# Kernel tuning notes

Hardware: AMD Instinct MI355X
Metric: run time of the kernel (lower is better)

Reference implementation:

```python
import jax, jax.numpy as jnp
import numpy as np

N_HEADS = 32
EPS = 1e-7
ROPE_BASE = 10000.0


def rms_norm(x, gamma):
    return x / jnp.sqrt(EPS + jnp.mean(x * x, axis=-1, keepdims=True)) * gamma


def rope_tables(seq_len, head_dim, dtype=jnp.float32):
    inv_freq = 1.0 / (ROPE_BASE ** (jnp.arange(0, head_dim, 2, dtype=jnp.float32) / head_dim))
    angles = jnp.arange(seq_len, dtype=jnp.float32)[:, None] * inv_freq[None, :]  # [S, D/2]
    angles = jnp.concatenate([angles, angles], axis=-1)  # [S, D]
    return jnp.cos(angles).astype(dtype), jnp.sin(angles).astype(dtype)


def apply_rope(x, cos, sin):
    # x: [B, H, S, D]; cos/sin: [S, D]
    d = x.shape[-1]
    x1, x2 = x[..., : d // 2], x[..., d // 2 :]
    rotated = jnp.concatenate([-x2, x1], axis=-1)
    return x * cos[None, None] + rotated * sin[None, None]


def setup_inputs() -> dict:
    key = jax.random.key(0)
    ks = jax.random.split(key, 9)
    B, S, D, Hd = 1, 2048, 4096, 11008
    s = lambda k, shape, fan: jax.random.normal(k, shape, jnp.float32) * (fan ** -0.5)
    return {
        "X": jax.random.normal(ks[0], (B, S, D), jnp.float32),
        "Wq": s(ks[1], (D, D), D),
        "Wk": s(ks[2], (D, D), D),
        "Wv": s(ks[3], (D, D), D),
        "Wo": s(ks[4], (D, D), D),
        "bo": jnp.zeros((D,), jnp.float32),
        "gamma1": jnp.ones((D,), jnp.float32),
        "gamma2": jnp.ones((D,), jnp.float32),
        "W1": s(ks[5], (D, Hd), D),
        "W2": s(ks[6], (D, Hd), D),
        "W3": s(ks[7], (Hd, D), Hd),
    }


def reference(X, Wq, Wk, Wv, Wo, bo, gamma1, gamma2, W1, W2, W3):
    B, S, D = X.shape
    H = N_HEADS
    hd = D // H

    # --- attention sublayer ---
    h = rms_norm(X, gamma1)
    q = (h @ Wq).reshape(B, S, H, hd).transpose(0, 2, 1, 3)  # [B,H,S,hd]
    k = (h @ Wk).reshape(B, S, H, hd).transpose(0, 2, 1, 3)
    v = (h @ Wv).reshape(B, S, H, hd).transpose(0, 2, 1, 3)

    cos, sin = rope_tables(S, hd, X.dtype)
    q = apply_rope(q, cos, sin)
    k = apply_rope(k, cos, sin)

    scores = jnp.einsum("bhsd,bhtd->bhst", q, k) / jnp.sqrt(jnp.asarray(hd, X.dtype))
    causal = jnp.tril(jnp.ones((S, S), bool))
    scores = jnp.where(causal, scores, -jnp.inf)
    attn = jax.nn.softmax(scores, axis=-1)
    out = jnp.einsum("bhst,bhtd->bhsd", attn, v)
    out = out.transpose(0, 2, 1, 3).reshape(B, S, D)
    out = out @ Wo + bo
    X = X + out

    # --- SwiGLU FFN sublayer ---
    h2 = rms_norm(X, gamma2)
    x1 = h2 @ W1
    x2 = h2 @ W2
    ff = (x1 * jax.nn.sigmoid(x1) * x2) @ W3
    return X + ff
```

## Files before the change

### kernel.cpp

```cpp
#include <hip/hip_runtime.h>
#include <hip/hip_bf16.h>
#include <cstdint>
#include <cmath>

typedef __bf16 bf16;
typedef __attribute__((ext_vector_type(8))) __bf16 bf16x8;
typedef __attribute__((ext_vector_type(4))) __bf16 bf16x4;
typedef __attribute__((ext_vector_type(4))) float f32x4;

__device__ __forceinline__ void gload_lds16(const void* g, void* l) {
  __builtin_amdgcn_global_load_lds((__attribute__((address_space(1))) void*)g,
                                   (__attribute__((address_space(3))) void*)l,
                                   16, 0, 0);
}

template<int EPI>
__global__ __launch_bounds__(512, 2) void gemmd(
    const bf16* __restrict__ A, const bf16* __restrict__ Bt, void* __restrict__ Cv,
    const float* __restrict__ cosT, const float* __restrict__ sinT,
    bf16* __restrict__ q_out, bf16* __restrict__ k_out, bf16* __restrict__ v_out,
    int M, int N, int K, int ksd, int gm) {
  extern __shared__ char lds[];
  constexpr int BM = 256;
  constexpr int ASZ = BM * 128;
  constexpr int BUFS = ASZ + 32768;
  constexpr int MF = 4;

  const int tid = threadIdx.x;
  const int wave = tid >> 6, lane = tid & 63;
  const int wr = wave >> 1, wc = wave & 1;
  const int l15 = lane & 15, l4 = lane >> 4;
  const int qq = gridDim.x >> 3;
  const int wgid = (blockIdx.x & 7) * qq + (blockIdx.x >> 3);
  const int tm = wgid % gm;
  int tq = wgid / gm;
  int split = 0;
  if (EPI == 5) { split = tq / (N >> 8); tq = tq % (N >> 8); }
  const int tn = tq;
  const long brow = (long)tm * BM, bcol = (long)tn * 256;
  const long koff = (long)split * K;
  const int NT = K >> 6;
  const bf16* Ab = A + brow * ksd + koff;
  const bf16* Bb = Bt + bcol * ksd + koff;

  f32x4 acc[MF][8];
  #pragma unroll
  for (int i = 0; i < MF; ++i)
    #pragma unroll
    for (int j = 0; j < 8; ++j) acc[i][j] = (f32x4){0.f, 0.f, 0.f, 0.f};

  bf16x8 a[MF][2], b[8][2];

  auto stage = [&](int T) {
    const long kofs = (long)T << 6;
    char* wb = lds + (T & 1) * BUFS;
    #pragma unroll
    for (int i = 0; i < 4; ++i) {
      const int slot = i * 512 + tid, r = slot >> 3, c0 = slot & 7;
      gload_lds16(Ab + (long)r * ksd + kofs + ((c0 ^ (r & 7)) << 3), wb + slot * 16);
    }
    #pragma unroll
    for (int i = 0; i < 4; ++i) {
      const int slot = i * 512 + tid, r = slot >> 3, c0 = slot & 7;
      gload_lds16(Bb + (long)r * ksd + kofs + ((c0 ^ (r & 7)) << 3), wb + ASZ + slot * 16);
    }
  };

  stage(0);
  __syncthreads();

  for (int g = 0; g < NT; ++g) {
    const int pg = (g & 1) * BUFS;
    if (g + 1 < NT) stage(g + 1);
    #pragma unroll
    for (int nf = 0; nf < 8; ++nf)
      #pragma unroll
      for (int ks = 0; ks < 2; ++ks) {
        const int r = wc * 128 + nf * 16 + l15;
        b[nf][ks] = *(const bf16x8*)(lds + pg + ASZ + r * 128 + (((ks * 4 + l4) ^ (r & 7)) << 4));
      }
    #pragma unroll
    for (int mf = 0; mf < MF; ++mf)
      #pragma unroll
      for (int ks = 0; ks < 2; ++ks) {
        const int r = wr * 64 + mf * 16 + l15;
        a[mf][ks] = *(const bf16x8*)(lds + pg + r * 128 + (((ks * 4 + l4) ^ (r & 7)) << 4));
      }
    #pragma unroll
    for (int ks = 0; ks < 2; ++ks)
      #pragma unroll
      for (int mf = 0; mf < MF; ++mf)
        #pragma unroll
        for (int nf = 0; nf < 8; ++nf)
          acc[mf][nf] = __builtin_amdgcn_mfma_f32_16x16x32_bf16(
              a[mf][ks], b[nf][ks], acc[mf][nf], 0, 0, 0);
    __syncthreads();
  }

  if (EPI == 5) {
    bf16* dst = (split == 0 ? q_out : v_out);
    #pragma unroll
    for (int mf = 0; mf < MF; ++mf) {
      const long row0 = brow + wr * 64 + mf * 16 + l4 * 4;
      #pragma unroll
      for (int nf = 0; nf < 8; ++nf) {
        const long col = bcol + wc * 128 + nf * 16 + l15;
        #pragma unroll
        for (int rj = 0; rj < 4; ++rj)
          dst[(row0 + rj) * N + col] = (bf16)acc[mf][nf][rj];
      }
    }
  } else if (EPI == 3) {
    const int region = (int)(bcol >> 12);
    const int hc = (int)(bcol & 4095) + wc * 128;
    const int h = hc >> 7;
    if (region < 2) {
      bf16* dh = (region == 0 ? q_out : k_out) + (long)h * 2048 * 128;
      #pragma unroll
      for (int mf = 0; mf < MF; ++mf) {
        #pragma unroll
        for (int rj = 0; rj < 4; ++rj) {
          const int s = (int)brow + wr * 64 + mf * 16 + l4 * 4 + rj;
          const float* cr = cosT + s * 64;
          const float* sr = sinT + s * 64;
          #pragma unroll
          for (int nfp = 0; nfp < 4; ++nfp) {
            const int d = nfp * 16 + l15;
            const float c = cr[d], sn = sr[d];
            const float x1 = acc[mf][nfp][rj], x2 = acc[mf][nfp + 4][rj];
            dh[(long)s * 128 + d]      = (bf16)(x1 * c - x2 * sn);
            dh[(long)s * 128 + d + 64] = (bf16)(x2 * c + x1 * sn);
          }
        }
      }
    } else {
      bf16* dh = v_out + (long)h * 128 * 2048;
      #pragma unroll
      for (int mf = 0; mf < MF; ++mf) {
        const int s0 = (int)brow + wr * 64 + mf * 16 + l4 * 4;
        #pragma unroll
        for (int nf = 0; nf < 8; ++nf) {
          const int d = nf * 16 + l15;
          bf16x4 v;
          #pragma unroll
          for (int rj = 0; rj < 4; ++rj) v[rj] = (bf16)acc[mf][nf][rj];
          *(bf16x4*)(dh + (long)d * 2048 + s0) = v;
        }
      }
    }
  } else if (EPI == 4) {
    #pragma unroll
    for (int mf = 0; mf < MF; ++mf) {
      #pragma unroll
      for (int rj = 0; rj < 4; ++rj) {
        const int s = (int)brow + wr * 64 + mf * 16 + l4 * 4 + rj;
        bf16* gr = (bf16*)Cv + (long)s * 11008;
        #pragma unroll
        for (int nfp = 0; nfp < 4; ++nfp) {
          const int col = (int)bcol + wc * 128 + nfp * 32 + l15;
          const int jj = ((col >> 5) << 4) + l15;
          const float x1 = acc[mf][2 * nfp][rj], x2 = acc[mf][2 * nfp + 1][rj];
          const float sg = x1 / (1.f + __expf(-x1));
          gr[jj] = (bf16)(sg * x2);
        }
      }
    }
  }
}

__global__ __launch_bounds__(256) void combine_kernel(
    const bf16* __restrict__ p0, const bf16* __restrict__ p1,
    const float* __restrict__ X2, float* __restrict__ out) {
  const long i = ((long)blockIdx.x * 256 + threadIdx.x) * 8;
  bf16x8 a = *(const bf16x8*)(p0 + i);
  bf16x8 b = *(const bf16x8*)(p1 + i);
  #pragma unroll
  for (int j = 0; j < 8; ++j)
    out[i + j] = (float)a[j] + (float)b[j] + X2[i + j];
}

__global__ __launch_bounds__(256) void combine_wo_kernel(
    const bf16* __restrict__ p0, const bf16* __restrict__ p1,
    const float* __restrict__ bo, const float* __restrict__ X,
    const float* __restrict__ g2, float* __restrict__ X2,
    bf16* __restrict__ h2) {
  const int row = blockIdx.x;
  const long base = (long)row * 4096;
  float v[16];
  float ss = 0.f;
  #pragma unroll
  for (int c = 0; c < 2; ++c) {
    const int col = threadIdx.x * 8 + c * 2048;
    bf16x8 a = *(const bf16x8*)(p0 + base + col);
    bf16x8 b = *(const bf16x8*)(p1 + base + col);
    #pragma unroll
    for (int j = 0; j < 8; ++j) {
      const float val = (float)a[j] + (float)b[j] + bo[col + j] + X[base + col + j];
      v[c * 8 + j] = val;
      ss += val * val;
      X2[base + col + j] = val;
    }
  }
  #pragma unroll
  for (int off = 32; off; off >>= 1) ss += __shfl_down(ss, off, 64);
  __shared__ float wsum[4];
  if ((threadIdx.x & 63) == 0) wsum[threadIdx.x >> 6] = ss;
  __syncthreads();
  const float tot = wsum[0] + wsum[1] + wsum[2] + wsum[3];
  const float scale = rsqrtf(1e-7f + tot / 4096.f);
  #pragma unroll
  for (int c = 0; c < 2; ++c) {
    const int col = threadIdx.x * 8 + c * 2048;
    bf16x8 o;
    #pragma unroll
    for (int j = 0; j < 8; ++j)
      o[j] = (bf16)(v[c * 8 + j] * scale * g2[col + j]);
    *(bf16x8*)(h2 + base + col) = o;
  }
}

__device__ __forceinline__ void trans64(
    const float* __restrict__ in, bf16* __restrict__ out,
    int R, int C, int bx, int by, int ilv, int off) {
  __shared__ float t[64][65];
  const int lr = threadIdx.x >> 4;
  const int lc4 = (threadIdx.x & 15) * 4;
  #pragma unroll
  for (int i = 0; i < 4; ++i) {
    const int r = lr + i * 16;
    const float4 v = *(const float4*)(in + (long)(by * 64 + r) * C + bx * 64 + lc4);
    t[r][lc4] = v.x; t[r][lc4 + 1] = v.y; t[r][lc4 + 2] = v.z; t[r][lc4 + 3] = v.w;
  }
  __syncthreads();
  const int oc = threadIdx.x >> 4;
  const int or4 = (threadIdx.x & 15) * 4;
  #pragma unroll
  for (int i = 0; i < 4; ++i) {
    const int c = oc + i * 16;
    const int j = bx * 64 + c;
    const int rdst = ilv ? (((j >> 4) << 5) + off + (j & 15)) : j;
    bf16x4 v;
    #pragma unroll
    for (int k = 0; k < 4; ++k) v[k] = (bf16)t[or4 + k][c];
    *(bf16x4*)(out + (long)rdst * R + by * 64 + or4) = v;
  }
}

__global__ __launch_bounds__(256) void prep_kernel(
    const float* __restrict__ Wq, const float* __restrict__ Wk,
    const float* __restrict__ Wv, const float* __restrict__ Wo,
    const float* __restrict__ W1, const float* __restrict__ W2,
    const float* __restrict__ W3, const float* __restrict__ X,
    const float* __restrict__ g1,
    bf16* __restrict__ WqkvT, bf16* __restrict__ WoT,
    bf16* __restrict__ W12T, bf16* __restrict__ W3T,
    float* __restrict__ cosT, float* __restrict__ sinT,
    bf16* __restrict__ hbuf) {
  const int bid = blockIdx.x;
  if (bid < 16384) {
    const int seg = bid >> 12, idx = bid & 4095;
    const float* in = (seg == 0 ? Wq : seg == 1 ? Wk : seg == 2 ? Wv : Wo);
    bf16* out = (seg == 3 ? WoT : WqkvT + (long)seg * 4096 * 4096);
    trans64(in, out, 4096, 4096, idx & 63, idx >> 6, 0, 0);
  } else if (bid < 38400) {
    const int idx = bid - 16384;
    const int seg = idx / 11008, li = idx % 11008;
    trans64(seg ? W2 : W1, W12T, 4096, 11008, li % 172, li / 172, 1, seg * 16);
  } else if (bid < 49408) {
    const int idx = bid - 38400;
    trans64(W3, W3T, 11008, 4096, idx & 63, idx >> 6, 0, 0);
  } else if (bid < 49920) {
    const int gidx = (bid - 49408) * 256 + threadIdx.x;
    const int i = gidx & 63, s = gidx >> 6;
    const float inv = powf(10000.f, -(float)i / 64.f);
    const float ang = (float)s * inv;
    cosT[gidx] = cosf(ang);
    sinT[gidx] = sinf(ang);
  } else {
    const int row = bid - 49920;
    const float* xr = X + (long)row * 4096;
    float ss = 0.f;
    for (int i = threadIdx.x * 4; i < 4096; i += 1024) {
      float4 v = *(const float4*)(xr + i);
      ss += v.x * v.x + v.y * v.y + v.z * v.z + v.w * v.w;
    }
    #pragma unroll
    for (int off = 32; off; off >>= 1) ss += __shfl_down(ss, off, 64);
    __shared__ float wsum[4];
    if ((threadIdx.x & 63) == 0) wsum[threadIdx.x >> 6] = ss;
    __syncthreads();
    const float tot = wsum[0] + wsum[1] + wsum[2] + wsum[3];
    const float scale = rsqrtf(1e-7f + tot / 4096.f);
    bf16* orow = hbuf + (long)row * 4096;
    for (int i = threadIdx.x * 4; i < 4096; i += 1024) {
      float4 v = *(const float4*)(xr + i);
      float4 g = *(const float4*)(g1 + i);
      orow[i]     = (bf16)(v.x * scale * g.x);
      orow[i + 1] = (bf16)(v.y * scale * g.y);
      orow[i + 2] = (bf16)(v.z * scale * g.z);
      orow[i + 3] = (bf16)(v.w * scale * g.w);
    }
  }
}

__global__ __launch_bounds__(256) void attn_kernel(
    const bf16* __restrict__ qh, const bf16* __restrict__ kh,
    const bf16* __restrict__ vt, bf16* __restrict__ outb) {
  constexpr int S = 2048;
  const int qb = blockIdx.x, head = blockIdx.y;
  const int tid = threadIdx.x, wave = tid >> 6, lane = tid & 63;
  __shared__ bf16 Ks[2][64 * 128];
  __shared__ bf16 Vs[2][128 * 64];
  __shared__ bf16 Plds[4][16 * 64];
  const bf16* qhh = qh + (long)head * S * 128;
  const bf16* khh = kh + (long)head * S * 128;
  const bf16* vth = vt + (long)head * 128 * S;

  const int l15 = lane & 15, l4 = lane >> 4;
  const int qrow = qb * 64 + wave * 16 + l15;
  bf16x8 qf[4];
  #pragma unroll
  for (int kf = 0; kf < 4; ++kf)
    qf[kf] = *(const bf16x8*)(qhh + (long)qrow * 128 + kf * 32 + l4 * 8);

  auto stageKV = [&](int tb, int buf) {
    #pragma unroll
    for (int i = 0; i < 4; ++i) {
      const int c = wave + 4 * i;
      const int krlow = (c & 3) * 4 + l4;
      gload_lds16(khh + (long)(tb * 64 + c * 4 + l4) * 128 + ((l15 ^ krlow) * 8),
                  Ks[buf] + c * 512);
      gload_lds16(vth + (long)(c * 8 + (lane >> 3)) * S + tb * 64 +
                      (((lane & 7) ^ (lane >> 3)) * 8),
                  Vs[buf] + c * 512);
    }
  };

  float m_r[4], l_r[4];
  #pragma unroll
  for (int r = 0; r < 4; ++r) { m_r[r] = -INFINITY; l_r[r] = 0.f; }
  f32x4 oacc[8] = {};
  const float scale = 0.08838834764831845f;

  stageKV(0, 0);
  __syncthreads();

  for (int tb = 0; tb <= qb; ++tb) {
    const int buf = tb & 1;
    if (tb < qb) stageKV(tb + 1, buf ^ 1);

    f32x4 sf[4];
    #pragma unroll
    for (int ft = 0; ft < 4; ++ft) {
      f32x4 acn = {};
      #pragma unroll
      for (int kf = 0; kf < 4; ++kf) {
        bf16x8 kfr = *(const bf16x8*)(Ks[buf] + (ft * 16 + l15) * 128 +
                                      (((kf * 4 + l4) ^ l15) * 8));
        acn = __builtin_amdgcn_mfma_f32_16x16x32_bf16(qf[kf], kfr, acn, 0, 0, 0);
      }
      #pragma unroll
      for (int r = 0; r < 4; ++r) sf[ft][r] = acn[r] * scale;
    }
    if (tb == qb) {
      #pragma unroll
      for (int ft = 0; ft < 4; ++ft) {
        const int t_l = ft * 16 + l15;
        #pragma unroll
        for (int r = 0; r < 4; ++r)
          if (t_l > wave * 16 + l4 * 4 + r) sf[ft][r] = -INFINITY;
      }
    }
    float scl[4];
    #pragma unroll
    for (int r = 0; r < 4; ++r) {
      float mx = fmaxf(fmaxf(sf[0][r], sf[1][r]), fmaxf(sf[2][r], sf[3][r]));
      mx = fmaxf(mx, __shfl_xor(mx, 1, 64));
      mx = fmaxf(mx, __shfl_xor(mx, 2, 64));
      mx = fmaxf(mx, __shfl_xor(mx, 4, 64));
      mx = fmaxf(mx, __shfl_xor(mx, 8, 64));
      const float mnew = fmaxf(m_r[r], mx);
      scl[r] = __expf(m_r[r] - mnew);
      m_r[r] = mnew;
      float rs = 0.f;
      #pragma unroll
      for (int ft = 0; ft < 4; ++ft) {
        const float pexp = __expf(sf[ft][r] - mnew);
        sf[ft][r] = pexp;
        rs += pexp;
      }
      rs += __shfl_xor(rs, 1, 64);
      rs += __shfl_xor(rs, 2, 64);
      rs += __shfl_xor(rs, 4, 64);
      rs += __shfl_xor(rs, 8, 64);
      l_r[r] = l_r[r] * scl[r] + rs;
    }
    #pragma unroll
    for (int ft = 0; ft < 4; ++ft)
      #pragma unroll
      for (int r = 0; r < 4; ++r) {
        const int q = l4 * 4 + r;
        const int sl = (ft * 2 + (l15 >> 3)) ^ (q & 7);
        Plds[wave][q * 64 + sl * 8 + (l15 & 7)] = (bf16)sf[ft][r];
      }
    #pragma unroll
    for (int fd = 0; fd < 8; ++fd)
      #pragma unroll
      for (int r = 0; r < 4; ++r) oacc[fd][r] *= scl[r];
    #pragma unroll
    for (int fd = 0; fd < 8; ++fd) {
      #pragma unroll
      for (int kt = 0; kt < 2; ++kt) {
        bf16x8 pa = *(const bf16x8*)(&Plds[wave][l15 * 64 +
                        (((kt * 4 + l4) ^ (l15 & 7)) * 8)]);
        bf16x8 vb = *(const bf16x8*)(Vs[buf] + (fd * 16 + l15) * 64 +
                        (((kt * 4 + l4) ^ (l15 & 7)) * 8));
        oacc[fd] = __builtin_amdgcn_mfma_f32_16x16x32_bf16(pa, vb, oacc[fd], 0, 0, 0);
      }
    }
    __syncthreads();
  }
  #pragma unroll
  for (int fd = 0; fd < 8; ++fd) {
    #pragma unroll
    for (int r = 0; r < 4; ++r) {
      const long row = qb * 64 + wave * 16 + l4 * 4 + r;
      outb[row * 4096 + head * 128 + fd * 16 + l15] = (bf16)(oacc[fd][r] / l_r[r]);
    }
  }
}

extern "C" void kernel_launch(void* const* d_in, const int* in_sizes, int n_in,
                              void* d_out, int out_size, void* d_ws, size_t ws_size,
                              hipStream_t stream) {
  const float* X  = (const float*)d_in[0];
  const float* Wq = (const float*)d_in[1];
  const float* Wk = (const float*)d_in[2];
  const float* Wv = (const float*)d_in[3];
  const float* Wo = (const float*)d_in[4];
  const float* bo = (const float*)d_in[5];
  const float* g1 = (const float*)d_in[6];
  const float* g2 = (const float*)d_in[7];
  const float* W1 = (const float*)d_in[8];
  const float* W2 = (const float*)d_in[9];
  const float* W3 = (const float*)d_in[10];
  float* out = (float*)d_out;

  hipFuncSetAttribute((const void*)gemmd<3>, hipFuncAttributeMaxDynamicSharedMemorySize, 131072);
  hipFuncSetAttribute((const void*)gemmd<4>, hipFuncAttributeMaxDynamicSharedMemorySize, 131072);
  hipFuncSetAttribute((const void*)gemmd<5>, hipFuncAttributeMaxDynamicSharedMemorySize, 131072);

  char* p = (char*)d_ws;
  auto alloc = [&](size_t bytes) {
    char* r = p;
    p += (bytes + 255) & ~(size_t)255;
    return r;
  };
  float* cosT = (float*)alloc(2048 * 64 * 4);
  float* sinT = (float*)alloc(2048 * 64 * 4);
  bf16* WqkvT = (bf16*)alloc(12288L * 4096 * 2);
  bf16* WoT  = (bf16*)alloc(4096L * 4096 * 2);
  bf16* W12T = (bf16*)alloc(22016L * 4096 * 2);
  bf16* W3T  = (bf16*)alloc(4096L * 11008 * 2);
  bf16* qhB  = (bf16*)alloc(2048L * 4096 * 2);
  bf16* khB  = (bf16*)alloc(2048L * 4096 * 2);
  bf16* vtB  = (bf16*)alloc(2048L * 4096 * 2);
  bf16* hbuf = (bf16*)alloc(2048L * 4096 * 2);
  bf16* h2   = (bf16*)alloc(2048L * 4096 * 2);
  float* X2  = (float*)alloc(2048L * 4096 * 4);

  bf16* gsw = (bf16*)WqkvT;
  bf16* attnb = hbuf;
  bf16* P0 = qhB;
  bf16* P1 = khB;

  prep_kernel<<<51968, 256, 0, stream>>>(Wq, Wk, Wv, Wo, W1, W2, W3, X, g1,
                                         WqkvT, WoT, W12T, W3T, cosT, sinT, hbuf);

  gemmd<3><<<384, 512, 131072, stream>>>(hbuf, WqkvT, nullptr,
                                         cosT, sinT, qhB, khB, vtB,
                                         2048, 12288, 4096, 4096, 8);

  attn_kernel<<<dim3(32, 32), 256, 0, stream>>>(qhB, khB, vtB, attnb);

  gemmd<5><<<256, 512, 131072, stream>>>(attnb, WoT, nullptr,
                                         nullptr, nullptr, P0, nullptr, P1,
                                         2048, 4096, 2048, 4096, 8);

  combine_wo_kernel<<<2048, 256, 0, stream>>>(P0, P1, bo, X, g2, X2, h2);

  gemmd<4><<<688, 512, 131072, stream>>>(h2, W12T, gsw,
                                         nullptr, nullptr, nullptr, nullptr, nullptr,
                                         2048, 22016, 4096, 4096, 8);

  gemmd<5><<<256, 512, 131072, stream>>>(gsw, W3T, nullptr,
                                         nullptr, nullptr, P0, nullptr, P1,
                                         2048, 4096, 5504, 11008, 8);

  combine_kernel<<<4096, 256, 0, stream>>>(P0, P1, X2, out);
}
```

Measured before the change: 1.190 ms.

## Switch Wo, W12 and W3 GEMMs to 32x32x16 MFMA tiles

Splits the QKV GEMM into its own kernel that keeps the 16x16x32 MFMA path with the RoPE epilogue. The Wo, gate/up and down-projection GEMMs move to a new kernel that uses 32x32x16 bf16 MFMA with f32x16 accumulators. The W1/W2 interleave in the weight prep changes from 16-column to 32-column groups so the SwiGLU epilogue lines up with the 32-wide fragment layout. The aim is fewer MFMA issues and fewer LDS fragment loads per unit of work. The trade-off is a different LDS read pattern and epilogue store layout that must still match the XOR swizzle.

```diff
diff --git a/kernel.cpp b/kernel.cpp
--- a/kernel.cpp
+++ b/kernel.cpp
@@ -7,6 +7,7 @@
 typedef __attribute__((ext_vector_type(8))) __bf16 bf16x8;
 typedef __attribute__((ext_vector_type(4))) __bf16 bf16x4;
 typedef __attribute__((ext_vector_type(4))) float f32x4;
+typedef __attribute__((ext_vector_type(16))) float f32x16;
 
 __device__ __forceinline__ void gload_lds16(const void* g, void* l) {
   __builtin_amdgcn_global_load_lds((__attribute__((address_space(1))) void*)g,
@@ -14,22 +15,133 @@
                                    16, 0, 0);
 }
 
-template<int EPI>
-__global__ __launch_bounds__(512, 2) void gemmd(
-    const bf16* __restrict__ A, const bf16* __restrict__ Bt, void* __restrict__ Cv,
+__global__ __launch_bounds__(512, 2) void qkv_gemm(
+    const bf16* __restrict__ A, const bf16* __restrict__ Bt,
     const float* __restrict__ cosT, const float* __restrict__ sinT,
     bf16* __restrict__ q_out, bf16* __restrict__ k_out, bf16* __restrict__ v_out,
-    int M, int N, int K, int ksd, int gm) {
+    int M, int N, int K, int gm) {
   extern __shared__ char lds[];
-  constexpr int BM = 256;
-  constexpr int ASZ = BM * 128;
+  constexpr int ASZ = 256 * 128;
   constexpr int BUFS = ASZ + 32768;
-  constexpr int MF = 4;
 
   const int tid = threadIdx.x;
   const int wave = tid >> 6, lane = tid & 63;
   const int wr = wave >> 1, wc = wave & 1;
   const int l15 = lane & 15, l4 = lane >> 4;
+  const int qq = gridDim.x >> 3;
+  const int wgid = (blockIdx.x & 7) * qq + (blockIdx.x >> 3);
+  const int tm = wgid % gm, tn = wgid / gm;
+  const long brow = (long)tm * 256, bcol = (long)tn * 256;
+  const int NT = K >> 6;
+  const bf16* Ab = A + brow * K;
+  const bf16* Bb = Bt + bcol * K;
+
+  f32x4 acc[4][8];
+  #pragma unroll
+  for (int i = 0; i < 4; ++i)
+    #pragma unroll
+    for (int j = 0; j < 8; ++j) acc[i][j] = (f32x4){0.f, 0.f, 0.f, 0.f};
+
+  bf16x8 a[4][2], b[8][2];
+
+  auto stage = [&](int T) {
+    const long kofs = (long)T << 6;
+    char* wb = lds + (T & 1) * BUFS;
+    #pragma unroll
+    for (int i = 0; i < 4; ++i) {
+      const int slot = i * 512 + tid, r = slot >> 3, c0 = slot & 7;
+      gload_lds16(Ab + (long)r * K + kofs + ((c0 ^ (r & 7)) << 3), wb + slot * 16);
+    }
+    #pragma unroll
+    for (int i = 0; i < 4; ++i) {
+      const int slot = i * 512 + tid, r = slot >> 3, c0 = slot & 7;
+      gload_lds16(Bb + (long)r * K + kofs + ((c0 ^ (r & 7)) << 3), wb + ASZ + slot * 16);
+    }
+  };
+
+  stage(0);
+  __syncthreads();
+
+  for (int g = 0; g < NT; ++g) {
+    const int pg = (g & 1) * BUFS;
+    if (g + 1 < NT) stage(g + 1);
+    #pragma unroll
+    for (int nf = 0; nf < 8; ++nf)
+      #pragma unroll
+      for (int ks = 0; ks < 2; ++ks) {
+        const int r = wc * 128 + nf * 16 + l15;
+        b[nf][ks] = *(const bf16x8*)(lds + pg + ASZ + r * 128 + (((ks * 4 + l4) ^ (r & 7)) << 4));
+      }
+    #pragma unroll
+    for (int mf = 0; mf < 4; ++mf)
+      #pragma unroll
+      for (int ks = 0; ks < 2; ++ks) {
+        const int r = wr * 64 + mf * 16 + l15;
+        a[mf][ks] = *(const bf16x8*)(lds + pg + r * 128 + (((ks * 4 + l4) ^ (r & 7)) << 4));
+      }
+    #pragma unroll
+    for (int ks = 0; ks < 2; ++ks)
+      #pragma unroll
+      for (int mf = 0; mf < 4; ++mf)
+        #pragma unroll
+        for (int nf = 0; nf < 8; ++nf)
+          acc[mf][nf] = __builtin_amdgcn_mfma_f32_16x16x32_bf16(
+              a[mf][ks], b[nf][ks], acc[mf][nf], 0, 0, 0);
+    __syncthreads();
+  }
+
+  const int region = (int)(bcol >> 12);
+  const int hc = (int)(bcol & 4095) + wc * 128;
+  const int h = hc >> 7;
+  if (region < 2) {
+    bf16* dh = (region == 0 ? q_out : k_out) + (long)h * 2048 * 128;
+    #pragma unroll
+    for (int mf = 0; mf < 4; ++mf) {
+      #pragma unroll
+      for (int rj = 0; rj < 4; ++rj) {
+        const int s = (int)brow + wr * 64 + mf * 16 + l4 * 4 + rj;
+        const float* cr = cosT + s * 64;
+        const float* sr = sinT + s * 64;
+        #pragma unroll
+        for (int nfp = 0; nfp < 4; ++nfp) {
+          const int d = nfp * 16 + l15;
+          const float c = cr[d], sn = sr[d];
+          const float x1 = acc[mf][nfp][rj], x2 = acc[mf][nfp + 4][rj];
+          dh[(long)s * 128 + d]      = (bf16)(x1 * c - x2 * sn);
+          dh[(long)s * 128 + d + 64] = (bf16)(x2 * c + x1 * sn);
+        }
+      }
+    }
+  } else {
+    bf16* dh = v_out + (long)h * 128 * 2048;
+    #pragma unroll
+    for (int mf = 0; mf < 4; ++mf) {
+      const int s0 = (int)brow + wr * 64 + mf * 16 + l4 * 4;
+      #pragma unroll
+      for (int nf = 0; nf < 8; ++nf) {
+        const int d = nf * 16 + l15;
+        bf16x4 v;
+        #pragma unroll
+        for (int rj = 0; rj < 4; ++rj) v[rj] = (bf16)acc[mf][nf][rj];
+        *(bf16x4*)(dh + (long)d * 2048 + s0) = v;
+      }
+    }
+  }
+}
+
+template<int EPI>
+__global__ __launch_bounds__(512, 2) void gemm32(
+    const bf16* __restrict__ A, const bf16* __restrict__ Bt, void* __restrict__ Cv,
+    bf16* __restrict__ p0_out, bf16* __restrict__ p1_out,
+    int M, int N, int K, int ksd, int gm) {
+  extern __shared__ char lds[];
+  constexpr int ASZ = 256 * 128;
+  constexpr int BUFS = ASZ + 32768;
+
+  const int tid = threadIdx.x;
+  const int wave = tid >> 6, lane = tid & 63;
+  const int wr = wave >> 1, wc = wave & 1;
+  const int l31 = lane & 31, h5 = lane >> 5;
   const int qq = gridDim.x >> 3;
   const int wgid = (blockIdx.x & 7) * qq + (blockIdx.x >> 3);
   const int tm = wgid % gm;
@@ -37,19 +149,21 @@
   int split = 0;
   if (EPI == 5) { split = tq / (N >> 8); tq = tq % (N >> 8); }
   const int tn = tq;
-  const long brow = (long)tm * BM, bcol = (long)tn * 256;
+  const long brow = (long)tm * 256, bcol = (long)tn * 256;
   const long koff = (long)split * K;
   const int NT = K >> 6;
   const bf16* Ab = A + brow * ksd + koff;
   const bf16* Bb = Bt + bcol * ksd + koff;
 
-  f32x4 acc[MF][8];
-  #pragma unroll
-  for (int i = 0; i < MF; ++i)
-    #pragma unroll
-    for (int j = 0; j < 8; ++j) acc[i][j] = (f32x4){0.f, 0.f, 0.f, 0.f};
-
-  bf16x8 a[MF][2], b[8][2];
+  f32x16 acc[2][4];
+  #pragma unroll
+  for (int i = 0; i < 2; ++i)
+    #pragma unroll
+    for (int j = 0; j < 4; ++j)
+      #pragma unroll
+      for (int e = 0; e < 16; ++e) acc[i][j][e] = 0.f;
+
+  bf16x8 a[2][4], b[4][4];
 
   auto stage = [&](int T) {
     const long kofs = (long)T << 6;
@@ -73,95 +187,59 @@
     const int pg = (g & 1) * BUFS;
     if (g + 1 < NT) stage(g + 1);
     #pragma unroll
-    for (int nf = 0; nf < 8; ++nf)
-      #pragma unroll
-      for (int ks = 0; ks < 2; ++ks) {
-        const int r = wc * 128 + nf * 16 + l15;
-        b[nf][ks] = *(const bf16x8*)(lds + pg + ASZ + r * 128 + (((ks * 4 + l4) ^ (r & 7)) << 4));
-      }
-    #pragma unroll
-    for (int mf = 0; mf < MF; ++mf)
-      #pragma unroll
-      for (int ks = 0; ks < 2; ++ks) {
-        const int r = wr * 64 + mf * 16 + l15;
-        a[mf][ks] = *(const bf16x8*)(lds + pg + r * 128 + (((ks * 4 + l4) ^ (r & 7)) << 4));
-      }
-    #pragma unroll
-    for (int ks = 0; ks < 2; ++ks)
-      #pragma unroll
-      for (int mf = 0; mf < MF; ++mf)
-        #pragma unroll
-        for (int nf = 0; nf < 8; ++nf)
-          acc[mf][nf] = __builtin_amdgcn_mfma_f32_16x16x32_bf16(
+    for (int nf = 0; nf < 4; ++nf)
+      #pragma unroll
+      for (int ks = 0; ks < 4; ++ks) {
+        const int r = wc * 128 + nf * 32 + l31;
+        b[nf][ks] = *(const bf16x8*)(lds + pg + ASZ + r * 128 + (((ks * 2 + h5) ^ (r & 7)) << 4));
+      }
+    #pragma unroll
+    for (int mf = 0; mf < 2; ++mf)
+      #pragma unroll
+      for (int ks = 0; ks < 4; ++ks) {
+        const int r = wr * 64 + mf * 32 + l31;
+        a[mf][ks] = *(const bf16x8*)(lds + pg + r * 128 + (((ks * 2 + h5) ^ (r & 7)) << 4));
+      }
+    #pragma unroll
+    for (int ks = 0; ks < 4; ++ks)
+      #pragma unroll
+      for (int mf = 0; mf < 2; ++mf)
+        #pragma unroll
+        for (int nf = 0; nf < 4; ++nf)
+          acc[mf][nf] = __builtin_amdgcn_mfma_f32_32x32x16_bf16(
               a[mf][ks], b[nf][ks], acc[mf][nf], 0, 0, 0);
     __syncthreads();
   }
 
   if (EPI == 5) {
-    bf16* dst = (split == 0 ? q_out : v_out);
-    #pragma unroll
-    for (int mf = 0; mf < MF; ++mf) {
-      const long row0 = brow + wr * 64 + mf * 16 + l4 * 4;
-      #pragma unroll
-      for (int nf = 0; nf < 8; ++nf) {
-        const long col = bcol + wc * 128 + nf * 16 + l15;
-        #pragma unroll
-        for (int rj = 0; rj < 4; ++rj)
-          dst[(row0 + rj) * N + col] = (bf16)acc[mf][nf][rj];
-      }
-    }
-  } else if (EPI == 3) {
-    const int region = (int)(bcol >> 12);
-    const int hc = (int)(bcol & 4095) + wc * 128;
-    const int h = hc >> 7;
-    if (region < 2) {
-      bf16* dh = (region == 0 ? q_out : k_out) + (long)h * 2048 * 128;
-      #pragma unroll
-      for (int mf = 0; mf < MF; ++mf) {
-        #pragma unroll
-        for (int rj = 0; rj < 4; ++rj) {
-          const int s = (int)brow + wr * 64 + mf * 16 + l4 * 4 + rj;
-          const float* cr = cosT + s * 64;
-          const float* sr = sinT + s * 64;
-          #pragma unroll
-          for (int nfp = 0; nfp < 4; ++nfp) {
-            const int d = nfp * 16 + l15;
-            const float c = cr[d], sn = sr[d];
-            const float x1 = acc[mf][nfp][rj], x2 = acc[mf][nfp + 4][rj];
-            dh[(long)s * 128 + d]      = (bf16)(x1 * c - x2 * sn);
-            dh[(long)s * 128 + d + 64] = (bf16)(x2 * c + x1 * sn);
-          }
+    bf16* dst = (split == 0 ? p0_out : p1_out);
+    #pragma unroll
+    for (int mf = 0; mf < 2; ++mf) {
+      const long row0 = brow + wr * 64 + mf * 32 + 4 * h5;
+      #pragma unroll
+      for (int nf = 0; nf < 4; ++nf) {
+        const long col = bcol + wc * 128 + nf * 32 + l31;
+        #pragma unroll
+        for (int reg = 0; reg < 16; ++reg) {
+          const long row = row0 + (reg & 3) + 8 * (reg >> 2);
+          dst[row * N + col] = (bf16)acc[mf][nf][reg];
         }
       }
-    } else {
-      bf16* dh = v_out + (long)h * 128 * 2048;
-      #pragma unroll
-      for (int mf = 0; mf < MF; ++mf) {
-        const int s0 = (int)brow + wr * 64 + mf * 16 + l4 * 4;
-        #pragma unroll
-        for (int nf = 0; nf < 8; ++nf) {
-          const int d = nf * 16 + l15;
-          bf16x4 v;
-          #pragma unroll
-          for (int rj = 0; rj < 4; ++rj) v[rj] = (bf16)acc[mf][nf][rj];
-          *(bf16x4*)(dh + (long)d * 2048 + s0) = v;
-        }
-      }
-    }
-  } else if (EPI == 4) {
-    #pragma unroll
-    for (int mf = 0; mf < MF; ++mf) {
-      #pragma unroll
-      for (int rj = 0; rj < 4; ++rj) {
-        const int s = (int)brow + wr * 64 + mf * 16 + l4 * 4 + rj;
-        bf16* gr = (bf16*)Cv + (long)s * 11008;
-        #pragma unroll
-        for (int nfp = 0; nfp < 4; ++nfp) {
-          const int col = (int)bcol + wc * 128 + nfp * 32 + l15;
-          const int jj = ((col >> 5) << 4) + l15;
-          const float x1 = acc[mf][2 * nfp][rj], x2 = acc[mf][2 * nfp + 1][rj];
+    }
+  } else {
+    #pragma unroll
+    for (int mf = 0; mf < 2; ++mf) {
+      const int s0 = (int)brow + wr * 64 + mf * 32 + 4 * h5;
+      #pragma unroll
+      for (int q = 0; q < 2; ++q) {
+        const int col = (int)bcol + wc * 128 + q * 64 + l31;
+        const int jj = ((col >> 6) << 5) + l31;
+        #pragma unroll
+        for (int reg = 0; reg < 16; ++reg) {
+          const int s = s0 + (reg & 3) + 8 * (reg >> 2);
+          const float x1 = acc[mf][2 * q][reg], x2 = acc[mf][2 * q + 1][reg];
           const float sg = x1 / (1.f + __expf(-x1));
-          gr[jj] = (bf16)(sg * x2);
+          ((bf16*)Cv)[(long)s * 11008 + jj] = (bf16)(sg * x2);
         }
       }
     }
@@ -238,7 +316,7 @@
   for (int i = 0; i < 4; ++i) {
     const int c = oc + i * 16;
     const int j = bx * 64 + c;
-    const int rdst = ilv ? (((j >> 4) << 5) + off + (j & 15)) : j;
+    const int rdst = ilv ? (((j >> 5) << 6) + off + (j & 31)) : j;
     bf16x4 v;
     #pragma unroll
     for (int k = 0; k < 4; ++k) v[k] = (bf16)t[or4 + k][c];
@@ -265,7 +343,7 @@
   } else if (bid < 38400) {
     const int idx = bid - 16384;
     const int seg = idx / 11008, li = idx % 11008;
-    trans64(seg ? W2 : W1, W12T, 4096, 11008, li % 172, li / 172, 1, seg * 16);
+    trans64(seg ? W2 : W1, W12T, 4096, 11008, li % 172, li / 172, 1, seg * 32);
   } else if (bid < 49408) {
     const int idx = bid - 38400;
     trans64(W3, W3T, 11008, 4096, idx & 63, idx >> 6, 0, 0);
@@ -446,9 +524,9 @@
   const float* W3 = (const float*)d_in[10];
   float* out = (float*)d_out;
 
-  hipFuncSetAttribute((const void*)gemmd<3>, hipFuncAttributeMaxDynamicSharedMemorySize, 131072);
-  hipFuncSetAttribute((const void*)gemmd<4>, hipFuncAttributeMaxDynamicSharedMemorySize, 131072);
-  hipFuncSetAttribute((const void*)gemmd<5>, hipFuncAttributeMaxDynamicSharedMemorySize, 131072);
+  hipFuncSetAttribute((const void*)qkv_gemm, hipFuncAttributeMaxDynamicSharedMemorySize, 131072);
+  hipFuncSetAttribute((const void*)gemm32<4>, hipFuncAttributeMaxDynamicSharedMemorySize, 131072);
+  hipFuncSetAttribute((const void*)gemm32<5>, hipFuncAttributeMaxDynamicSharedMemorySize, 131072);
 
   char* p = (char*)d_ws;
   auto alloc = [&](size_t bytes) {
@@ -477,25 +555,22 @@
   prep_kernel<<<51968, 256, 0, stream>>>(Wq, Wk, Wv, Wo, W1, W2, W3, X, g1,
                                          WqkvT, WoT, W12T, W3T, cosT, sinT, hbuf);
 
-  gemmd<3><<<384, 512, 131072, stream>>>(hbuf, WqkvT, nullptr,
+  qkv_gemm<<<384, 512, 131072, stream>>>(hbuf, WqkvT,
                                          cosT, sinT, qhB, khB, vtB,
-                                         2048, 12288, 4096, 4096, 8);
+                                         2048, 12288, 4096, 8);
 
   attn_kernel<<<dim3(32, 32), 256, 0, stream>>>(qhB, khB, vtB, attnb);
 
-  gemmd<5><<<256, 512, 131072, stream>>>(attnb, WoT, nullptr,
-                                         nullptr, nullptr, P0, nullptr, P1,
-                                         2048, 4096, 2048, 4096, 8);
+  gemm32<5><<<256, 512, 131072, stream>>>(attnb, WoT, nullptr, P0, P1,
+                                          2048, 4096, 2048, 4096, 8);
 
   combine_wo_kernel<<<2048, 256, 0, stream>>>(P0, P1, bo, X, g2, X2, h2);
 
-  gemmd<4><<<688, 512, 131072, stream>>>(h2, W12T, gsw,
-                                         nullptr, nullptr, nullptr, nullptr, nullptr,
-                                         2048, 22016, 4096, 4096, 8);
-
-  gemmd<5><<<256, 512, 131072, stream>>>(gsw, W3T, nullptr,
-                                         nullptr, nullptr, P0, nullptr, P1,
-                                         2048, 4096, 5504, 11008, 8);
+  gemm32<4><<<688, 512, 131072, stream>>>(h2, W12T, gsw, nullptr, nullptr,
+                                          2048, 22016, 4096, 4096, 8);
+
+  gemm32<5><<<256, 512, 131072, stream>>>(gsw, W3T, nullptr, P0, P1,
+                                          2048, 4096, 5504, 11008, 8);
 
   combine_kernel<<<4096, 256, 0, stream>>>(P0, P1, X2, out);
 }
```

New measurement: 1.247 ms. 1.05x slower.
